# Kernel optimization log

Hardware: AMD Instinct MI355X
Metric: run time of the kernel (lower is better)

Reference implementation:

```python
import jax, jax.numpy as jnp
import numpy as np

B, T, C = 2, 2048, 2048
H, KVH, D = 16, 4, 128       # n_head, num_kv_heads, head_size
G = H // KVH                  # kv groups
SCALE = D ** -0.5
THETA = 10000.0


def setup_inputs() -> dict:
    key = jax.random.key(0)
    ks = jax.random.split(key, 5)
    s = 0.02
    return {
        "x": jax.random.normal(ks[0], (B, T, C), dtype=jnp.float32),
        "Wq": jax.random.normal(ks[1], (C, C), dtype=jnp.float32) * s,
        "bq": jnp.zeros((C,), jnp.float32),
        "Wk": jax.random.normal(ks[2], (C, KVH * D), dtype=jnp.float32) * s,
        "bk": jnp.zeros((KVH * D,), jnp.float32),
        "Wv": jax.random.normal(ks[3], (C, KVH * D), dtype=jnp.float32) * s,
        "bv": jnp.zeros((KVH * D,), jnp.float32),
        "Wo": jax.random.normal(ks[4], (C, C), dtype=jnp.float32) * s,
        "bo": jnp.zeros((C,), jnp.float32),
    }


def _rope(x):
    # x: [B, h, T, D]; interleaved-pair RoPE (lucidrains rotary-embedding-torch style)
    half = D // 2
    inv_freq = 1.0 / (THETA ** (jnp.arange(0, D, 2, dtype=jnp.float32) / D))  # [half]
    t = jnp.arange(T, dtype=jnp.float32)
    ang = t[:, None] * inv_freq[None, :]                 # [T, half]
    cos = jnp.repeat(jnp.cos(ang), 2, axis=-1)           # [T, D]
    sin = jnp.repeat(jnp.sin(ang), 2, axis=-1)
    xp = x.reshape(*x.shape[:-1], half, 2)
    x_rot = jnp.stack([-xp[..., 1], xp[..., 0]], axis=-1).reshape(x.shape)
    return x * cos + x_rot * sin


def reference(x, Wq, bq, Wk, bk, Wv, bv, Wo, bo):
    # projections
    q = (x @ Wq + bq).reshape(B, T, H, D).transpose(0, 2, 1, 3)      # [B,H,T,D]
    k = (x @ Wk + bk).reshape(B, T, KVH, D).transpose(0, 2, 1, 3)    # [B,KVH,T,D]
    v = (x @ Wv + bv).reshape(B, T, KVH, D).transpose(0, 2, 1, 3)
    # RoPE pre-attention
    q = _rope(q)
    k = _rope(k)
    # GQA: group query heads against shared KV heads (no repeat materialization)
    qg = q.reshape(B, KVH, G, T, D)
    att = jnp.einsum("bhgtd,bhsd->bhgts", qg, k) * SCALE              # [B,KVH,G,T,T]
    causal = jnp.tril(jnp.ones((T, T), dtype=bool))
    att = jnp.where(causal, att, jnp.float32(-jnp.inf))
    att = jax.nn.softmax(att, axis=-1)
    y = jnp.einsum("bhgts,bhsd->bhgtd", att, v)                        # [B,KVH,G,T,D]
    y = y.reshape(B, H, T, D).transpose(0, 2, 1, 3).reshape(B, T, C)
    return y @ Wo + bo
```

## Files before the change

kernel.cpp:

```cpp
#include <hip/hip_runtime.h>
#include <hip/hip_bf16.h>

typedef __bf16 bf16;
typedef __attribute__((ext_vector_type(8))) __bf16 bf16x8;
typedef __attribute__((ext_vector_type(4))) float f32x4;

#define SCALE_QK 0.08838834764831845f
#define SCALE2   (0.08838834764831845f * 1.4426950408889634f)

__device__ inline void gload16(const bf16* g, bf16* l) {
  __builtin_amdgcn_global_load_lds((const __attribute__((address_space(1))) void*)g,
                                   (__attribute__((address_space(3))) void*)l, 16, 0, 0);
}

__global__ void cvt_kernel(const float* __restrict__ in, bf16* __restrict__ out, int n8) {
  int i = blockIdx.x * 256 + threadIdx.x;
  if (i >= n8) return;
  const float* p = in + (size_t)i * 8;
  float4 a = *(const float4*)p, b = *(const float4*)(p + 4);
  union { uint4 u; bf16 h[8]; } un;
  un.h[0] = (bf16)a.x; un.h[1] = (bf16)a.y; un.h[2] = (bf16)a.z; un.h[3] = (bf16)a.w;
  un.h[4] = (bf16)b.x; un.h[5] = (bf16)b.y; un.h[6] = (bf16)b.z; un.h[7] = (bf16)b.w;
  *(uint4*)(out + (size_t)i * 8) = un.u;
}

__global__ void concat_bias_kernel(const float* __restrict__ bq, const float* __restrict__ bk,
                                   const float* __restrict__ bv, float* __restrict__ o) {
  int i = blockIdx.x * 256 + threadIdx.x;
  if (i >= 3072) return;
  o[i] = (i < 2048) ? bq[i] : (i < 2560 ? bk[i - 2048] : bv[i - 2560]);
}

__global__ __launch_bounds__(256)
void transpose_cvt_kernel(const float* __restrict__ in, bf16* __restrict__ out, int K, int N) {
  __shared__ bf16 tile[64][72];
  int n0 = blockIdx.x * 64, k0 = blockIdx.y * 64;
  int t = threadIdx.x;
  int r8 = t >> 5, c2 = (t & 31) * 2;
#pragma unroll
  for (int it = 0; it < 8; it++) {
    int row = it * 8 + r8;
    float2 v = *(const float2*)(in + (size_t)(k0 + row) * N + n0 + c2);
    tile[row][c2] = (bf16)v.x;
    tile[row][c2 + 1] = (bf16)v.y;
  }
  __syncthreads();
  int r = t >> 3, c = (t & 7) * 8;
  int rot = t & 7;
#pragma unroll
  for (int it = 0; it < 2; it++) {
    int rr = it * 32 + r;
    union { uint4 u; bf16 h[8]; } un;
#pragma unroll
    for (int j = 0; j < 8; j++) {
      int jj = (j + rot) & 7;
      un.h[jj] = tile[c + jj][rr];
    }
    *(uint4*)(out + (size_t)(n0 + rr) * K + k0 + c) = un.u;
  }
}

__global__ __launch_bounds__(256)
void transpose_v_kernel(const bf16* __restrict__ qkv, bf16* __restrict__ vT) {
  __shared__ bf16 tile[64][72];
  int z = blockIdx.z;
  int b = z >> 2, kvh = z & 3;
  int d0 = blockIdx.y * 64;
  int t0 = blockIdx.x * 64;
  const bf16* in = qkv + (size_t)(b * 2048) * 3072 + 2560 + kvh * 128;
  int t = threadIdx.x;
  int r = t >> 3, c = (t & 7) * 8;
#pragma unroll
  for (int it = 0; it < 2; it++) {
    int rr = it * 32 + r;
    *(uint4*)&tile[rr][c] = *(const uint4*)(in + (size_t)(t0 + rr) * 3072 + d0 + c);
  }
  __syncthreads();
  int rot = t & 7;
#pragma unroll
  for (int it = 0; it < 2; it++) {
    int rr = it * 32 + r;
    union { uint4 u; bf16 h[8]; } un;
#pragma unroll
    for (int j = 0; j < 8; j++) {
      int jj = (j + rot) & 7;
      un.h[jj] = tile[c + jj][rr];
    }
    *(uint4*)(vT + (size_t)(z * 128 + d0 + rr) * 2048 + t0 + c) = un.u;
  }
}

__global__ void rope_table_kernel(float* __restrict__ cost, float* __restrict__ sint) {
  int idx = blockIdx.x * 256 + threadIdx.x;
  int t = idx >> 6, i = idx & 63;
  float inv = expf(-(float)i * (logf(10000.f) / 64.f));
  float ang = (float)t * inv;
  cost[idx] = cosf(ang);
  sint[idx] = sinf(ang);
}

__global__ void rope_apply_kernel(bf16* __restrict__ qkv, const float* __restrict__ cost,
                                  const float* __restrict__ sint) {
  int p = blockIdx.x * 256 + threadIdx.x;
  if (p >= 4096 * 320) return;
  int row = p / 320;
  int rc = p - row * 320;
  int e = rc * 8;
  int t = row & 2047;
  int i0 = (e & 127) >> 1;
  bf16* ptr = qkv + (size_t)row * 3072 + e;
  float4 cv = *(const float4*)(cost + t * 64 + i0);
  float4 sv = *(const float4*)(sint + t * 64 + i0);
  float c[4] = {cv.x, cv.y, cv.z, cv.w}, s[4] = {sv.x, sv.y, sv.z, sv.w};
  union { uint4 u; bf16 h[8]; } un;
  un.u = *(const uint4*)ptr;
#pragma unroll
  for (int j = 0; j < 4; j++) {
    float x0 = (float)un.h[2 * j], x1 = (float)un.h[2 * j + 1];
    un.h[2 * j]     = (bf16)(x0 * c[j] - x1 * s[j]);
    un.h[2 * j + 1] = (bf16)(x1 * c[j] + x0 * s[j]);
  }
  *(uint4*)ptr = un.u;
}

template <typename OutT>
__global__ __launch_bounds__(256)
void gemm_bias_kernel(const bf16* __restrict__ A, const bf16* __restrict__ Bt,
                      const float* __restrict__ bias, OutT* __restrict__ C,
                      int M, int N, int K, int lda, int ldc) {
  __shared__ bf16 As[2][128 * 64];
  __shared__ bf16 Bs[2][128 * 64];
  int tid = threadIdx.x;
  int wv = tid >> 6, l = tid & 63;
  int wr = wv >> 1, wc = wv & 1;
  int lr = l & 15, g = l >> 4;
  int m0 = blockIdx.y * 128, n0 = blockIdx.x * 128;

  auto stage = [&](int k0, int buf) {
#pragma unroll
    for (int i = 0; i < 4; i++) {
      int e = i * 256 + tid;
      int row = e >> 3, c = e & 7;
      int csrc = (c ^ (row & 7)) * 8;
      gload16(A + (size_t)(m0 + row) * lda + k0 + csrc, &As[buf][(size_t)e * 8]);
      gload16(Bt + (size_t)(n0 + row) * K + k0 + csrc, &Bs[buf][(size_t)e * 8]);
    }
  };

  f32x4 acc[4][4] = {};
  stage(0, 0);
  __syncthreads();
  int cur = 0;
  for (int k0 = 64; k0 <= K; k0 += 64) {
    if (k0 < K) stage(k0, cur ^ 1);
#pragma unroll
    for (int kk = 0; kk < 2; kk++) {
      int cmem = ((kk * 4 + g) ^ (lr & 7)) * 8;
      bf16x8 a[4], b[4];
#pragma unroll
      for (int mi = 0; mi < 4; mi++)
        a[mi] = *(const bf16x8*)&As[cur][(size_t)(wr * 64 + mi * 16 + lr) * 64 + cmem];
#pragma unroll
      for (int nj = 0; nj < 4; nj++)
        b[nj] = *(const bf16x8*)&Bs[cur][(size_t)(wc * 64 + nj * 16 + lr) * 64 + cmem];
#pragma unroll
      for (int mi = 0; mi < 4; mi++)
#pragma unroll
        for (int nj = 0; nj < 4; nj++)
          acc[mi][nj] = __builtin_amdgcn_mfma_f32_16x16x32_bf16(a[mi], b[nj], acc[mi][nj], 0, 0, 0);
    }
    __syncthreads();
    cur ^= 1;
  }
#pragma unroll
  for (int nj = 0; nj < 4; nj++) {
    int gc = n0 + wc * 64 + nj * 16 + lr;
    float bv = bias[gc];
#pragma unroll
    for (int mi = 0; mi < 4; mi++) {
      int gr = m0 + wr * 64 + mi * 16 + g * 4;
#pragma unroll
      for (int reg = 0; reg < 4; reg++)
        C[(size_t)(gr + reg) * ldc + gc] = (OutT)(acc[mi][nj][reg] + bv);
    }
  }
}

__global__ __launch_bounds__(256)
void attn_kernel(const bf16* __restrict__ qkv, const bf16* __restrict__ vT,
                 bf16* __restrict__ ybuf) {
  __shared__ bf16 Ks[2][64 * 128];
  __shared__ bf16 Vts[2][128 * 64];
  __shared__ bf16 Ps[4][16][72];

  int pair = blockIdx.x;
  int bh = blockIdx.y;
  int b = bh >> 4, h = bh & 15;
  int kvh = h >> 2;
  int tid = threadIdx.x, w = tid >> 6, l = tid & 63;
  int lr = l & 15, g = l >> 4, lk = g * 8;

  const bf16* kbase = qkv + (size_t)(b * 2048) * 3072 + 2048 + kvh * 128;
  const bf16* vtb   = vT + (size_t)(b * 4 + kvh) * 128 * 2048;
  f32x4 zero4 = {0.f, 0.f, 0.f, 0.f};

  auto stage = [&](int kv0, int buf) {
#pragma unroll
    for (int it = 0; it < 4; it++) {
      int cidx = it * 256 + tid;
      {
        int row = cidx >> 4, c = cidx & 15, csrc = c ^ (row & 7);
        gload16(kbase + (size_t)(kv0 + row) * 3072 + csrc * 8, &Ks[buf][(size_t)cidx * 8]);
      }
      {
        int row = cidx >> 3, c = cidx & 7, csrc = c ^ (row & 7);
        gload16(vtb + (size_t)row * 2048 + kv0 + csrc * 8, &Vts[buf][(size_t)cidx * 8]);
      }
    }
  };

  for (int half = 0; half < 2; half++) {
    int qt = half == 0 ? 31 - pair : pair;
    int q0 = qt * 64;

    const bf16* qbase = qkv + (size_t)(b * 2048 + q0 + w * 16 + lr) * 3072 + h * 128;
    bf16x8 qf[4];
#pragma unroll
    for (int kk = 0; kk < 4; kk++) qf[kk] = *(const bf16x8*)(qbase + kk * 32 + lk);

    float m_r = -1e30f, l_r = 0.f;
    f32x4 o_acc[8];
#pragma unroll
    for (int f = 0; f < 8; f++) o_acc[f] = zero4;

    stage(0, 0);
    __syncthreads();
    int cur = 0;

    for (int kvt = 0; kvt <= qt; kvt++) {
      if (kvt < qt) stage((kvt + 1) * 64, cur ^ 1);

      const bf16* ksCur = Ks[cur];
      f32x4 sa[4];
#pragma unroll
      for (int nj = 0; nj < 4; nj++) sa[nj] = zero4;
#pragma unroll
      for (int kk = 0; kk < 4; kk++) {
        int cmem = (kk * 4 + g) ^ (lr & 7);
#pragma unroll
        for (int nj = 0; nj < 4; nj++) {
          bf16x8 kf = *(const bf16x8*)&ksCur[(size_t)((nj * 16 + lr) * 16 + cmem) * 8];
          sa[nj] = __builtin_amdgcn_mfma_f32_16x16x32_bf16(kf, qf[kk], sa[nj], 0, 0, 0);
        }
      }

      bool diag = (kvt == qt);
      int qpos = w * 16 + lr;
      float p[4][4];
#pragma unroll
      for (int nj = 0; nj < 4; nj++)
#pragma unroll
        for (int rg = 0; rg < 4; rg++) {
          float s = sa[nj][rg] * SCALE2;
          if (diag && (nj * 16 + g * 4 + rg > qpos)) s = -1e30f;
          p[nj][rg] = s;
        }

      float a0 = fmaxf(fmaxf(p[0][0], p[0][1]), fmaxf(p[0][2], p[0][3]));
      float a1 = fmaxf(fmaxf(p[1][0], p[1][1]), fmaxf(p[1][2], p[1][3]));
      float a2 = fmaxf(fmaxf(p[2][0], p[2][1]), fmaxf(p[2][2], p[2][3]));
      float a3 = fmaxf(fmaxf(p[3][0], p[3][1]), fmaxf(p[3][2], p[3][3]));
      float mx = fmaxf(fmaxf(a0, a1), fmaxf(a2, a3));
      mx = fmaxf(mx, __shfl_xor(mx, 16));
      mx = fmaxf(mx, __shfl_xor(mx, 32));
      float mnew = fmaxf(m_r, mx);
      float sc = exp2f(m_r - mnew);
#pragma unroll
      for (int nj = 0; nj < 4; nj++)
#pragma unroll
        for (int rg = 0; rg < 4; rg++) p[nj][rg] = exp2f(p[nj][rg] - mnew);
      float s0 = (p[0][0] + p[0][1]) + (p[0][2] + p[0][3]);
      float s1 = (p[1][0] + p[1][1]) + (p[1][2] + p[1][3]);
      float s2 = (p[2][0] + p[2][1]) + (p[2][2] + p[2][3]);
      float s3 = (p[3][0] + p[3][1]) + (p[3][2] + p[3][3]);
      float rs = (s0 + s1) + (s2 + s3);
      rs += __shfl_xor(rs, 16);
      rs += __shfl_xor(rs, 32);
      l_r = l_r * sc + rs;
      m_r = mnew;

      float osc[4];
#pragma unroll
      for (int rg = 0; rg < 4; rg++) osc[rg] = __shfl(sc, g * 4 + rg);
#pragma unroll
      for (int f = 0; f < 8; f++)
#pragma unroll
        for (int rg = 0; rg < 4; rg++) o_acc[f][rg] *= osc[rg];

#pragma unroll
      for (int nj = 0; nj < 4; nj++) {
        union { uint2 u; bf16 hh[4]; } pw;
#pragma unroll
        for (int rg = 0; rg < 4; rg++) pw.hh[rg] = (bf16)p[nj][rg];
        *(uint2*)&Ps[w][lr][nj * 16 + g * 4] = pw.u;
      }
      asm volatile("s_waitcnt lgkmcnt(0)" ::: "memory");
      __builtin_amdgcn_sched_barrier(0);

      const bf16* vtCur = Vts[cur];
#pragma unroll
      for (int kk2 = 0; kk2 < 2; kk2++) {
        bf16x8 pf = *(const bf16x8*)&Ps[w][lr][kk2 * 32 + lk];
        int cmem = (kk2 * 4 + g) ^ (lr & 7);
#pragma unroll
        for (int f = 0; f < 8; f++) {
          bf16x8 vf = *(const bf16x8*)&vtCur[(size_t)((f * 16 + lr) * 8 + cmem) * 8];
          o_acc[f] = __builtin_amdgcn_mfma_f32_16x16x32_bf16(pf, vf, o_acc[f], 0, 0, 0);
        }
      }
      __syncthreads();
      cur ^= 1;
    }

    float linv[4];
#pragma unroll
    for (int rg = 0; rg < 4; rg++) linv[rg] = 1.0f / __shfl(l_r, g * 4 + rg);
    size_t orow = (size_t)(b * 2048 + q0 + w * 16);
#pragma unroll
    for (int rg = 0; rg < 4; rg++) {
      int r = g * 4 + rg;
#pragma unroll
      for (int f = 0; f < 8; f++) {
        float ov = o_acc[f][rg] * linv[rg];
        ybuf[(orow + r) * 2048 + h * 128 + f * 16 + lr] = (bf16)ov;
      }
    }
    __syncthreads();
  }
}

extern "C" void kernel_launch(void* const* d_in, const int* in_sizes, int n_in,
                              void* d_out, int out_size, void* d_ws, size_t ws_size,
                              hipStream_t stream) {
  const float* x  = (const float*)d_in[0];
  const float* Wq = (const float*)d_in[1];
  const float* bq = (const float*)d_in[2];
  const float* Wk = (const float*)d_in[3];
  const float* bk = (const float*)d_in[4];
  const float* Wv = (const float*)d_in[5];
  const float* bv = (const float*)d_in[6];
  const float* Wo = (const float*)d_in[7];
  const float* bo = (const float*)d_in[8];
  float* out = (float*)d_out;

  char* w = (char*)d_ws;
  auto alloc = [&](size_t bytes) { char* p = w; w += (bytes + 255) & ~(size_t)255; return p; };
  bf16*  xb    = (bf16*)alloc((size_t)4096 * 2048 * 2);
  bf16*  wqkvT = (bf16*)alloc((size_t)3072 * 2048 * 2);
  bf16*  qkv   = (bf16*)alloc((size_t)4096 * 3072 * 2);
  bf16*  vTg   = (bf16*)alloc((size_t)8 * 128 * 2048 * 2);
  float* bqkv  = (float*)alloc((size_t)3072 * 4);
  float* cost  = (float*)alloc((size_t)2048 * 64 * 4);
  float* sint  = (float*)alloc((size_t)2048 * 64 * 4);
  bf16*  ybuf  = xb;
  bf16*  woT   = wqkvT;

  cvt_kernel<<<4096, 256, 0, stream>>>(x, xb, 4096 * 2048 / 8);
  concat_bias_kernel<<<12, 256, 0, stream>>>(bq, bk, bv, bqkv);
  transpose_cvt_kernel<<<dim3(32, 32), 256, 0, stream>>>(Wq, wqkvT, 2048, 2048);
  transpose_cvt_kernel<<<dim3(8, 32), 256, 0, stream>>>(Wk, wqkvT + (size_t)2048 * 2048, 2048, 512);
  transpose_cvt_kernel<<<dim3(8, 32), 256, 0, stream>>>(Wv, wqkvT + (size_t)2560 * 2048, 2048, 512);
  rope_table_kernel<<<512, 256, 0, stream>>>(cost, sint);
  gemm_bias_kernel<bf16><<<dim3(24, 32), 256, 0, stream>>>(xb, wqkvT, bqkv, qkv, 4096, 3072, 2048, 2048, 3072);
  transpose_cvt_kernel<<<dim3(32, 32), 256, 0, stream>>>(Wo, woT, 2048, 2048);
  transpose_v_kernel<<<dim3(32, 2, 8), 256, 0, stream>>>(qkv, vTg);
  rope_apply_kernel<<<5120, 256, 0, stream>>>(qkv, cost, sint);
  attn_kernel<<<dim3(16, 32), 256, 0, stream>>>(qkv, vTg, ybuf);
  gemm_bias_kernel<float><<<dim3(16, 32), 256, 0, stream>>>(ybuf, woT, bo, out, 4096, 2048, 2048, 2048, 2048);
}
```

Baseline: 297.2 us.

## Fuse RoPE into QKV GEMM epilogue and add lazy softmax rescaling

Applies the RoPE rotation inside the QKV projection GEMM epilogue, getting each element's pair partner from the neighbouring lane with a shuffle, and removes the separate rope_apply pass over q and k. The attention kernel now updates the running max and rescales the output accumulator only when some row's block max exceeds the stored max by more than 8 in log2 space, so most tiles skip the rescale multiplies. The epilogue gains scattered per-element loads from the cos/sin tables. The lazy rescale lets exponentials reach up to 2^8, which is safe in fp32 but adds a warp vote and a branch.

```diff
diff --git a/kernel.cpp b/kernel.cpp
--- a/kernel.cpp
+++ b/kernel.cpp
@@ -99,34 +99,11 @@
   sint[idx] = sinf(ang);
 }
 
-__global__ void rope_apply_kernel(bf16* __restrict__ qkv, const float* __restrict__ cost,
-                                  const float* __restrict__ sint) {
-  int p = blockIdx.x * 256 + threadIdx.x;
-  if (p >= 4096 * 320) return;
-  int row = p / 320;
-  int rc = p - row * 320;
-  int e = rc * 8;
-  int t = row & 2047;
-  int i0 = (e & 127) >> 1;
-  bf16* ptr = qkv + (size_t)row * 3072 + e;
-  float4 cv = *(const float4*)(cost + t * 64 + i0);
-  float4 sv = *(const float4*)(sint + t * 64 + i0);
-  float c[4] = {cv.x, cv.y, cv.z, cv.w}, s[4] = {sv.x, sv.y, sv.z, sv.w};
-  union { uint4 u; bf16 h[8]; } un;
-  un.u = *(const uint4*)ptr;
-#pragma unroll
-  for (int j = 0; j < 4; j++) {
-    float x0 = (float)un.h[2 * j], x1 = (float)un.h[2 * j + 1];
-    un.h[2 * j]     = (bf16)(x0 * c[j] - x1 * s[j]);
-    un.h[2 * j + 1] = (bf16)(x1 * c[j] + x0 * s[j]);
-  }
-  *(uint4*)ptr = un.u;
-}
-
-template <typename OutT>
+template <typename OutT, bool ROPE>
 __global__ __launch_bounds__(256)
 void gemm_bias_kernel(const bf16* __restrict__ A, const bf16* __restrict__ Bt,
                       const float* __restrict__ bias, OutT* __restrict__ C,
+                      const float* __restrict__ cost, const float* __restrict__ sint,
                       int M, int N, int K, int lda, int ldc) {
   __shared__ bf16 As[2][128 * 64];
   __shared__ bf16 Bs[2][128 * 64];
@@ -176,12 +153,24 @@
   for (int nj = 0; nj < 4; nj++) {
     int gc = n0 + wc * 64 + nj * 16 + lr;
     float bv = bias[gc];
+    bool doRope = ROPE && (gc < 2560);
+    int ti = (gc & 127) >> 1;
+    float sgn = (gc & 1) ? 1.f : -1.f;
 #pragma unroll
     for (int mi = 0; mi < 4; mi++) {
       int gr = m0 + wr * 64 + mi * 16 + g * 4;
 #pragma unroll
-      for (int reg = 0; reg < 4; reg++)
-        C[(size_t)(gr + reg) * ldc + gc] = (OutT)(acc[mi][nj][reg] + bv);
+      for (int reg = 0; reg < 4; reg++) {
+        float v = acc[mi][nj][reg] + bv;
+        float pv = __shfl_xor(v, 1);
+        if (doRope) {
+          int t = (gr + reg) & 2047;
+          float c = cost[t * 64 + ti];
+          float s = sint[t * 64 + ti];
+          v = v * c + sgn * pv * s;
+        }
+        C[(size_t)(gr + reg) * ldc + gc] = (OutT)v;
+      }
     }
   }
 }
@@ -273,12 +262,25 @@
       float mx = fmaxf(fmaxf(a0, a1), fmaxf(a2, a3));
       mx = fmaxf(mx, __shfl_xor(mx, 16));
       mx = fmaxf(mx, __shfl_xor(mx, 32));
-      float mnew = fmaxf(m_r, mx);
-      float sc = exp2f(m_r - mnew);
+
+      if (__any(mx > m_r + 8.0f)) {
+        float mnew = fmaxf(m_r, mx);
+        float sc = exp2f(m_r - mnew);
+        l_r *= sc;
+        m_r = mnew;
+        float osc[4];
+#pragma unroll
+        for (int rg = 0; rg < 4; rg++) osc[rg] = __shfl(sc, g * 4 + rg);
+#pragma unroll
+        for (int f = 0; f < 8; f++)
+#pragma unroll
+          for (int rg = 0; rg < 4; rg++) o_acc[f][rg] *= osc[rg];
+      }
+
 #pragma unroll
       for (int nj = 0; nj < 4; nj++)
 #pragma unroll
-        for (int rg = 0; rg < 4; rg++) p[nj][rg] = exp2f(p[nj][rg] - mnew);
+        for (int rg = 0; rg < 4; rg++) p[nj][rg] = exp2f(p[nj][rg] - m_r);
       float s0 = (p[0][0] + p[0][1]) + (p[0][2] + p[0][3]);
       float s1 = (p[1][0] + p[1][1]) + (p[1][2] + p[1][3]);
       float s2 = (p[2][0] + p[2][1]) + (p[2][2] + p[2][3]);
@@ -286,16 +288,7 @@
       float rs = (s0 + s1) + (s2 + s3);
       rs += __shfl_xor(rs, 16);
       rs += __shfl_xor(rs, 32);
-      l_r = l_r * sc + rs;
-      m_r = mnew;
-
-      float osc[4];
-#pragma unroll
-      for (int rg = 0; rg < 4; rg++) osc[rg] = __shfl(sc, g * 4 + rg);
-#pragma unroll
-      for (int f = 0; f < 8; f++)
-#pragma unroll
-        for (int rg = 0; rg < 4; rg++) o_acc[f][rg] *= osc[rg];
+      l_r += rs;
 
 #pragma unroll
       for (int nj = 0; nj < 4; nj++) {
@@ -371,10 +364,11 @@
   transpose_cvt_kernel<<<dim3(8, 32), 256, 0, stream>>>(Wk, wqkvT + (size_t)2048 * 2048, 2048, 512);
   transpose_cvt_kernel<<<dim3(8, 32), 256, 0, stream>>>(Wv, wqkvT + (size_t)2560 * 2048, 2048, 512);
   rope_table_kernel<<<512, 256, 0, stream>>>(cost, sint);
-  gemm_bias_kernel<bf16><<<dim3(24, 32), 256, 0, stream>>>(xb, wqkvT, bqkv, qkv, 4096, 3072, 2048, 2048, 3072);
+  gemm_bias_kernel<bf16, true><<<dim3(24, 32), 256, 0, stream>>>(
+      xb, wqkvT, bqkv, qkv, cost, sint, 4096, 3072, 2048, 2048, 3072);
   transpose_cvt_kernel<<<dim3(32, 32), 256, 0, stream>>>(Wo, woT, 2048, 2048);
   transpose_v_kernel<<<dim3(32, 2, 8), 256, 0, stream>>>(qkv, vTg);
-  rope_apply_kernel<<<5120, 256, 0, stream>>>(qkv, cost, sint);
   attn_kernel<<<dim3(16, 32), 256, 0, stream>>>(qkv, vTg, ybuf);
-  gemm_bias_kernel<float><<<dim3(16, 32), 256, 0, stream>>>(ybuf, woT, bo, out, 4096, 2048, 2048, 2048, 2048);
-}
+  gemm_bias_kernel<float, false><<<dim3(16, 32), 256, 0, stream>>>(
+      ybuf, woT, bo, out, nullptr, nullptr, 4096, 2048, 2048, 2048, 2048);
+}
```

Result: slower. 309.3 us (+4.1%).
